# Performance work log

Measured on AMD Instinct MI355X. Metric: run time of the kernel, lower is better.

The kernel has to match this reference:

```python
import jax, jax.numpy as jnp
import numpy as np
from jax import lax

C, CMID, RED, SCALE, KUP, KENC = 128, 64, 8, 2, 5, 3


def _conv(x, w, b=None, pad=0, groups=1):
    y = lax.conv_general_dilated(x, w, (1, 1), [(pad, pad), (pad, pad)],
                                 feature_group_count=groups,
                                 dimension_numbers=('NCHW', 'OIHW', 'NCHW'))
    if b is not None:
        y = y + b[None, :, None, None]
    return y


def setup_inputs() -> dict:
    key = jax.random.key(0)
    ks = jax.random.split(key, 8)
    s = 0.05
    return {
        'X': jax.random.normal(ks[0], (2, C, 64, 64), jnp.float32),
        'w3': jax.random.normal(ks[1], (CMID, C, 3, 3), jnp.float32) * s,
        'b3': jnp.zeros((CMID,), jnp.float32),
        'w5': jax.random.normal(ks[2], (CMID, C, 5, 5), jnp.float32) * s,
        'b5': jnp.zeros((CMID,), jnp.float32),
        'wa1': jax.random.normal(ks[3], (CMID // RED, CMID, 1, 1), jnp.float32) * s,
        'ba1': jnp.zeros((CMID // RED,), jnp.float32),
        'wa2': jax.random.normal(ks[4], (CMID, CMID // RED, 1, 1), jnp.float32) * s,
        'ba2': jnp.zeros((CMID,), jnp.float32),
        'wedge': jax.random.normal(ks[5], (CMID, 1, 3, 3), jnp.float32) * s,
        'wenc': jax.random.normal(ks[6], ((SCALE * KUP) ** 2, CMID, KENC, KENC), jnp.float32) * s,
    }


def reference(X, w3, b3, w5, b5, wa1, ba1, wa2, ba2, wedge, wenc):
    b, c, h, w = X.shape
    h_, w_ = h * SCALE, w * SCALE

    # kernel-prediction branch: 3x3 + 5x5 compression convs
    W = _conv(X, w3, b3, pad=1) + _conv(X, w5, b5, pad=2)

    # DetailEnhanceAttention: SE-style channel gate + depthwise edge conv
    avg = jnp.mean(W, axis=(2, 3), keepdims=True)            # (b, cmid, 1, 1)
    a = _conv(avg, wa1, ba1, pad=0)
    a = jax.nn.sigmoid(_conv(a, wa2, ba2, pad=0))
    edge = _conv(W, wedge, None, pad=1, groups=CMID)          # depthwise 3x3
    W = W * a + edge

    # encoder conv -> (b, (scale*k_up)^2, h, w)
    W = _conv(W, wenc, None, pad=KENC // 2)

    # PixelShuffle(scale): channels (k_up^2, r, r) -> (k_up^2, h*r, w*r)
    Wp = W.reshape(b, KUP * KUP, SCALE, SCALE, h, w)
    Wp = Wp.transpose(0, 1, 4, 2, 5, 3).reshape(b, KUP * KUP, h_, w_)
    Wp = jax.nn.softmax(Wp, axis=1)                           # softmax over k_up^2 taps

    # nearest upsample of X to (b, c, h_, w_)
    Xu = jnp.repeat(jnp.repeat(X, SCALE, axis=2), SCALE, axis=3)

    # unfold: kernel=k_up, dilation=scale, padding=k_up//2*scale
    p = (KUP // 2) * SCALE
    Xpad = jnp.pad(Xu, ((0, 0), (0, 0), (p, p), (p, p)))
    # (b, c, k_up^2, h_, w_), tap index = ki*k_up + kj (torch unfold order)
    patches = jnp.stack([
        Xpad[:, :, i * SCALE:i * SCALE + h_, j * SCALE:j * SCALE + w_]
        for i in range(KUP) for j in range(KUP)
    ], axis=2)

    out = jnp.einsum('bkhw,bckhw->bchw', Wp, patches)
    return out
```

## Files before the change

### kernel.cpp

```cpp
#include <hip/hip_runtime.h>
#include <math.h>

typedef __attribute__((ext_vector_type(2))) _Float16 f16x2;
typedef __attribute__((ext_vector_type(4))) _Float16 f16x4;
typedef __attribute__((ext_vector_type(8))) _Float16 f16x8;
typedef __attribute__((ext_vector_type(4))) float f32x4;

#if __has_builtin(__builtin_amdgcn_fdot2)
#define FDOT2(a, b, c) __builtin_amdgcn_fdot2((a), (b), (c), false)
#else
static __device__ __forceinline__ float FDOT2(f16x2 a, f16x2 b, float c) {
  return c + (float)a[0] * (float)b[0] + (float)a[1] * (float)b[1];
}
#endif

#define XPAD8_B  0
#define WFC_B    2506752
#define WFE_B    2916352
#define WFEATP_B 3045376
#define WEDGET_B 4194304
#define BCOMB_B  4195456
#define AVG_B    4195712

__global__ __launch_bounds__(256) void prep_kernel(
    const float* __restrict__ X,
    const float* __restrict__ w3, const float* __restrict__ b3,
    const float* __restrict__ w5, const float* __restrict__ b5,
    const float* __restrict__ wedge, const float* __restrict__ wenc,
    char* __restrict__ wsb) {
  int idx = blockIdx.x * 256 + threadIdx.x;
  if (idx < 156672) {
    int x = idx % 72;
    int t = idx / 72;
    int y = t % 68;
    int t2 = t / 68;
    int gg = t2 & 15, b = t2 >> 4;
    int yy = y - 2, xx = x - 2;
    bool ok = (yy >= 0 && yy < 64 && xx >= 0 && xx < 64);
    f16x8 h;
#pragma unroll
    for (int j = 0; j < 8; ++j) {
      float v = ok ? X[((b * 128 + gg * 8 + j) << 12) + yy * 64 + xx] : 0.f;
      h[j] = (_Float16)v;
    }
    ((f16x8*)(wsb + XPAD8_B))[idx] = h;
  }
  if (idx < 25600) {
    int l = idx & 63;
    int q = idx >> 6;
    int ntg = q & 3;
    int q2 = q >> 2;
    int cc = q2 & 3;
    int t = q2 >> 2;
    int ky = t / 5, kx = t % 5;
    int oc = ntg * 16 + (l & 15);
    int ci0 = cc * 32 + (l >> 4) * 8;
    f16x8 h;
#pragma unroll
    for (int i = 0; i < 8; ++i) {
      int ci = ci0 + i;
      float v = w5[(oc * 128 + ci) * 25 + t];
      if (ky >= 1 && ky <= 3 && kx >= 1 && kx <= 3)
        v += w3[(oc * 128 + ci) * 9 + (ky - 1) * 3 + (kx - 1)];
      h[i] = (_Float16)v;
    }
    ((f16x8*)(wsb + WFC_B))[idx] = h;
  }
  if (idx < 8064) {
    int l = idx & 63;
    int q = idx >> 6;
    int nt = q % 7;
    int q2 = q / 7;
    int cc = q2 & 1;
    int t = q2 >> 1;
    int oc = nt * 16 + (l & 15);
    int ci0 = cc * 32 + (l >> 4) * 8;
    f16x8 h;
#pragma unroll
    for (int i = 0; i < 8; ++i) {
      float v = (oc < 100) ? wenc[(oc * 64 + ci0 + i) * 9 + t] : 0.f;
      h[i] = (_Float16)v;
    }
    ((f16x8*)(wsb + WFE_B))[idx] = h;
  }
  if (idx < 6272) {
    int plane = idx / 392, p = idx % 392;
    int r, c;
    if (p < 136) {
      r = (p >= 68) ? 65 : 0;
      c = p % 68;
    } else {
      int q = p - 136;
      r = 1 + (q >> 2);
      int cm = q & 3;
      c = (cm == 0) ? 0 : (64 + cm);
    }
    f16x8 z = {(_Float16)0.f, (_Float16)0.f, (_Float16)0.f, (_Float16)0.f,
               (_Float16)0.f, (_Float16)0.f, (_Float16)0.f, (_Float16)0.f};
    *(f16x8*)((_Float16*)(wsb + WFEATP_B) + ((size_t)(plane * 66 + r) * 68 + c) * 8) = z;
  }
  if (idx < 72) {
    int k = idx >> 3, gg = idx & 7;
    f16x8 h;
#pragma unroll
    for (int j = 0; j < 8; ++j) h[j] = (_Float16)wedge[(gg * 8 + j) * 9 + k];
    ((f16x8*)(wsb + WEDGET_B))[idx] = h;
  }
  if (idx < 64) ((float*)(wsb + BCOMB_B))[idx] = b3[idx] + b5[idx];
  if (idx < 128) ((float*)(wsb + AVG_B))[idx] = b3[idx & 63] + b5[idx & 63];
}

__global__ __launch_bounds__(256) void convw_kernel(
    const _Float16* __restrict__ xpad8, const f16x8* __restrict__ wfc,
    const float* __restrict__ bcomb, _Float16* __restrict__ wfeatp,
    float* __restrict__ avg) {
  __shared__ __attribute__((aligned(16))) _Float16 xs[16 * 776];
  __shared__ float red[2][64][4];
  __shared__ float redm[2][16];
  const int tid = threadIdx.x;
  const int z = blockIdx.z;
  const int b = z >> 2, ntg = z & 3;
  const int tx0 = blockIdx.x * 8, ty0 = blockIdx.y * 4;

  for (int u = tid; u < 1536; u += 256) {
    int gg = u / 96;
    int rem = u - gg * 96;
    int r = rem / 12, c = rem - r * 12;
    f16x8 v = *(const f16x8*)&xpad8[((size_t)((b * 16 + gg) * 68 + ty0 + r) * 72 + tx0 + c) * 8];
    *(f16x8*)&xs[gg * 776 + r * 96 + c * 8] = v;
  }
  __syncthreads();

  const int w = __builtin_amdgcn_readfirstlane(tid >> 6);
  const int l = tid & 63;
  const int pg = w & 1, kh = w >> 1;
  const int lm = l & 15, lg = l >> 4;
  const int p = pg * 16 + lm;
  const int abase = (p >> 3) * 96 + (p & 7) * 8;

  f32x4 acc = {0.f, 0.f, 0.f, 0.f};
  for (int dy = 0; dy < 5; ++dy) {
    for (int dx = 0; dx < 5; ++dx) {
      const int t = dy * 5 + dx;
      const int toff = abase + dy * 96 + dx * 8;
#pragma unroll
      for (int cc2 = 0; cc2 < 2; ++cc2) {
        const int cc = kh * 2 + cc2;
        f16x8 a = *(const f16x8*)&xs[(cc * 4 + lg) * 776 + toff];
        f16x8 bb = wfc[((t * 4 + cc) * 4 + ntg) * 64 + l];
        acc = __builtin_amdgcn_mfma_f32_16x16x32_f16(a, bb, acc, 0, 0, 0);
      }
    }
  }

  if (kh == 1) {
#pragma unroll
    for (int r = 0; r < 4; ++r) red[pg][l][r] = acc[r];
  }
  __syncthreads();
  if (kh == 0) {
#pragma unroll
    for (int r = 0; r < 4; ++r) acc[r] += red[pg][l][r];
    float s = acc[0] + acc[1] + acc[2] + acc[3];
    s += __shfl_xor(s, 16);
    s += __shfl_xor(s, 32);
    if (lg == 0) redm[pg][lm] = s;
    const float bias = bcomb[ntg * 16 + lm];
#pragma unroll
    for (int r = 0; r < 4; ++r) {
      int pd = pg * 16 + lg * 4 + r;
      xs[pd * 24 + lm] = (_Float16)(acc[r] + bias);
    }
  }
  __syncthreads();
  if (tid < 64) {
    int pd = tid >> 1, g2 = tid & 1;
    f16x8 v = *(const f16x8*)&xs[pd * 24 + g2 * 8];
    int gy = ty0 + (pd >> 3), gx = tx0 + (pd & 7);
    *(f16x8*)&wfeatp[((size_t)((b * 8 + ntg * 2 + g2) * 66 + 1 + gy) * 68 + 1 + gx) * 8] = v;
  }
  if (tid < 16) {
    float tot = redm[0][tid] + redm[1][tid];
    atomicAdd(&avg[b * 64 + ntg * 16 + tid], tot * (1.f / 4096.f));
  }
}

#define SM_XT  0
#define SM_XSV 19968
#define SM_TS  25216
#define SM_SML 25216
#define SM_SMW 32640
#define SM_WED 36480
#define SM_TLA 37632
#define SM_GSH 37664
#define SM_TOT 37920

__global__ __launch_bounds__(512) void enccarafe_kernel(
    const _Float16* __restrict__ wfeatp, const f16x8* __restrict__ wfe,
    const _Float16* __restrict__ xpad8, const f16x8* __restrict__ wedgeT,
    const float* __restrict__ wa1, const float* __restrict__ ba1,
    const float* __restrict__ wa2, const float* __restrict__ ba2,
    const float* __restrict__ avg, float* __restrict__ out) {
  __shared__ __attribute__((aligned(16))) char smem[SM_TOT];
  _Float16* xt = (_Float16*)(smem + SM_XT);
  _Float16* xsv = (_Float16*)(smem + SM_XSV);
  _Float16* ts = (_Float16*)(smem + SM_TS);
  float* sml = (float*)(smem + SM_SML);
  f16x2* smw2 = (f16x2*)(smem + SM_SMW);
  f16x8* wedt = (f16x8*)(smem + SM_WED);
  float* tlat = (float*)(smem + SM_TLA);
  float* gsh = (float*)(smem + SM_GSH);

  const int tid = threadIdx.x;
  const int b = blockIdx.z;
  const int tx0 = blockIdx.x * 8, ty0 = blockIdx.y * 2;

  for (int u = tid; u < 1248; u += 512) {
    int gg = u / 78;
    int rem = u - gg * 78;
    int r = rem / 13, c = rem - r * 13;
    f16x8 v = *(const f16x8*)&xpad8[((size_t)((b * 16 + gg) * 68 + ty0 + r) * 72 + tx0 + c) * 8];
    *(f16x8*)&xt[gg * 624 + r * 104 + c * 8] = v;
  }
  for (int u = tid; u < 576; u += 512) {
    int gg = u / 72;
    int rem = u - gg * 72;
    int r = rem / 12, c = rem - r * 12;
    int pr = ty0 - 1 + r, pc = tx0 - 1 + c;
    f16x8 v = {(_Float16)0.f, (_Float16)0.f, (_Float16)0.f, (_Float16)0.f,
               (_Float16)0.f, (_Float16)0.f, (_Float16)0.f, (_Float16)0.f};
    if (pr >= 0 && pr < 66 && pc >= 0 && pc < 68)
      v = *(const f16x8*)&wfeatp[((size_t)((b * 8 + gg) * 66 + pr) * 68 + pc) * 8];
    *(f16x8*)&ts[gg * 584 + r * 96 + c * 8] = v;
  }
  if (tid < 72) wedt[tid] = wedgeT[tid];
  if (tid < 8) {
    float s = ba1[tid];
    for (int i = 0; i < 64; ++i) s += wa1[tid * 64 + i] * avg[b * 64 + i];
    tlat[tid] = s;
  }
  __syncthreads();
  if (tid < 64) {
    float s = ba2[tid];
#pragma unroll
    for (int j = 0; j < 8; ++j) s += wa2[tid * 8 + j] * tlat[j];
    gsh[tid] = 1.f / (1.f + expf(-s));
  }
  __syncthreads();

  if (tid < 320) {
    int gg = tid / 40;
    int rem = tid - gg * 40;
    int r6 = rem / 10, c10 = rem - r6 * 10;
    int vy = ty0 - 1 + r6, vx = tx0 - 1 + c10;
    f16x8 res = {(_Float16)0.f, (_Float16)0.f, (_Float16)0.f, (_Float16)0.f,
                 (_Float16)0.f, (_Float16)0.f, (_Float16)0.f, (_Float16)0.f};
    if (vy >= 0 && vy < 64 && vx >= 0 && vx < 64) {
      float vout[8];
      f16x8 ctr = *(const f16x8*)&ts[gg * 584 + (r6 + 1) * 96 + (c10 + 1) * 8];
#pragma unroll
      for (int j = 0; j < 8; ++j) vout[j] = (float)ctr[j] * gsh[gg * 8 + j];
#pragma unroll
      for (int ky = 0; ky < 3; ++ky) {
#pragma unroll
        for (int kx = 0; kx < 3; ++kx) {
          int k = ky * 3 + kx;
          f16x8 tv = *(const f16x8*)&ts[gg * 584 + (r6 + ky) * 96 + (c10 + kx) * 8];
          f16x8 wv = wedt[k * 8 + gg];
#pragma unroll
          for (int j = 0; j < 8; ++j) vout[j] = fmaf((float)wv[j], (float)tv[j], vout[j]);
        }
      }
#pragma unroll
      for (int j = 0; j < 8; ++j) res[j] = (_Float16)vout[j];
    }
    *(f16x8*)&xsv[gg * 328 + r6 * 80 + c10 * 8] = res;
  }
  __syncthreads();

  {
    const int w = __builtin_amdgcn_readfirstlane(tid >> 6);
    const int l = tid & 63;
    if (w < 7) {
      const int nt = w;
      const int lm = l & 15, lg = l >> 4;
      const int abase = (lm >> 3) * 80 + (lm & 7) * 8;

      f32x4 a0 = {0.f, 0.f, 0.f, 0.f};
      for (int dy = 0; dy < 3; ++dy) {
        for (int dx = 0; dx < 3; ++dx) {
          const int t = dy * 3 + dx;
          const int toff = abase + dy * 80 + dx * 8;
#pragma unroll
          for (int cc = 0; cc < 2; ++cc) {
            f16x8 a = *(const f16x8*)&xsv[(cc * 4 + lg) * 328 + toff];
            f16x8 b0 = wfe[((t * 2 + cc) * 7 + nt) * 64 + l];
            a0 = __builtin_amdgcn_mfma_f32_16x16x32_f16(a, b0, a0, 0, 0, 0);
          }
        }
      }
#pragma unroll
      for (int r = 0; r < 4; ++r)
        sml[(4 * lg + r) * 116 + nt * 16 + lm] = a0[r];
    }
  }
  __syncthreads();

  if (tid < 64) {
    int pix = tid >> 2, sub = tid & 3;
    float lv[25];
    float m = -1e30f;
#pragma unroll
    for (int k = 0; k < 25; ++k) {
      lv[k] = sml[pix * 116 + k * 4 + sub];
      m = fmaxf(m, lv[k]);
    }
    float s = 0.f;
#pragma unroll
    for (int k = 0; k < 25; ++k) {
      lv[k] = __expf(lv[k] - m);
      s += lv[k];
    }
    float inv = 1.f / s;
#pragma unroll
    for (int ki = 0; ki < 5; ++ki) {
#pragma unroll
      for (int pr = 0; pr < 3; ++pr) {
        float wlo = lv[ki * 5 + 2 * pr] * inv;
        float whi = (2 * pr + 1 < 5) ? lv[ki * 5 + 2 * pr + 1] * inv : 0.f;
        f16x2 pk = {(_Float16)wlo, (_Float16)whi};
        smw2[((ki * 3 + pr) * 16 + pix) * 4 + sub] = pk;
      }
    }
  }
  __syncthreads();

  {
    const int slot = tid >> 5;
    const int rem = tid & 31;
    const int syh = rem >> 4, pix = rem & 15;
    const int py = pix >> 3, px = pix & 7;
    const _Float16* xb = xt + slot * 624;

    float acc[2][8];
#pragma unroll
    for (int s = 0; s < 2; ++s)
#pragma unroll
      for (int j = 0; j < 8; ++j) acc[s][j] = 0.f;

    union U8 { f16x8 v; unsigned int u[4]; };
#pragma unroll
    for (int ki = 0; ki < 5; ++ki) {
      const _Float16* row = xb + (py + ki) * 104 + px * 8;
      U8 C[6];
#pragma unroll
      for (int c = 0; c < 6; ++c) C[c].v = *(const f16x8*)(row + c * 8);
#pragma unroll
      for (int pr = 0; pr < 3; ++pr) {
        const f16x2* wp = &smw2[((ki * 3 + pr) * 16 + pix) * 4 + syh * 2];
        f16x2 w0 = wp[0], w1 = wp[1];
        const U8& A = C[2 * pr];
        const U8& B = C[2 * pr + 1];
#pragma unroll
        for (int k = 0; k < 4; ++k) {
          unsigned int lo = __builtin_amdgcn_perm(B.u[k], A.u[k], 0x05040100u);
          unsigned int hi = __builtin_amdgcn_perm(B.u[k], A.u[k], 0x07060302u);
          f16x2 xlo = __builtin_bit_cast(f16x2, lo);
          f16x2 xhi = __builtin_bit_cast(f16x2, hi);
          acc[0][2 * k] = FDOT2(w0, xlo, acc[0][2 * k]);
          acc[1][2 * k] = FDOT2(w1, xlo, acc[1][2 * k]);
          acc[0][2 * k + 1] = FDOT2(w0, xhi, acc[0][2 * k + 1]);
          acc[1][2 * k + 1] = FDOT2(w1, xhi, acc[1][2 * k + 1]);
        }
      }
    }
    int y0o = 2 * (ty0 + py) + syh, x0o = 2 * (tx0 + px);
#pragma unroll
    for (int j = 0; j < 8; ++j) {
      int c = slot * 8 + j;
      float* op = out + ((size_t)(b * 128 + c) * 128 + y0o) * 128 + x0o;
      float2 v0 = {acc[0][j], acc[1][j]};
      *(float2*)op = v0;
    }
  }
}

extern "C" void kernel_launch(void* const* d_in, const int* in_sizes, int n_in,
                              void* d_out, int out_size, void* d_ws, size_t ws_size,
                              hipStream_t stream) {
  const float* X     = (const float*)d_in[0];
  const float* w3    = (const float*)d_in[1];
  const float* b3    = (const float*)d_in[2];
  const float* w5    = (const float*)d_in[3];
  const float* b5    = (const float*)d_in[4];
  const float* wa1   = (const float*)d_in[5];
  const float* ba1   = (const float*)d_in[6];
  const float* wa2   = (const float*)d_in[7];
  const float* ba2   = (const float*)d_in[8];
  const float* wedge = (const float*)d_in[9];
  const float* wenc  = (const float*)d_in[10];
  char* wsb = (char*)d_ws;
  float* out = (float*)d_out;

  _Float16* xpad8  = (_Float16*)(wsb + XPAD8_B);
  f16x8*    wfc    = (f16x8*)(wsb + WFC_B);
  f16x8*    wfe    = (f16x8*)(wsb + WFE_B);
  _Float16* wfeatp = (_Float16*)(wsb + WFEATP_B);
  f16x8*    wedgeT = (f16x8*)(wsb + WEDGET_B);
  float*    bcomb  = (float*)(wsb + BCOMB_B);
  float*    avg    = (float*)(wsb + AVG_B);

  prep_kernel<<<612, 256, 0, stream>>>(X, w3, b3, w5, b5, wedge, wenc, wsb);
  convw_kernel<<<dim3(8, 16, 8), 256, 0, stream>>>(xpad8, wfc, bcomb, wfeatp, avg);
  enccarafe_kernel<<<dim3(8, 32, 2), 512, 0, stream>>>(
      wfeatp, wfe, xpad8, wedgeT, wa1, ba1, wa2, ba2, avg, out);
}
```

Baseline: 42.16 us.

## Split enccarafe blocks across output channel halves with 256 threads each

The final fused encoder+CARAFE kernel now launches twice as many blocks of 256 threads, each handling half of the 128 output channels (cq selects which 64). Each block stages only its half of the padded X tile in shared memory, which cuts LDS usage and should allow more resident blocks. In exchange the edge/attention prologue and the encoder MFMA convolution plus softmax are computed redundantly in both channel-half blocks, and each wave now runs two MFMA accumulators.

```diff
diff --git a/kernel.cpp b/kernel.cpp
--- a/kernel.cpp
+++ b/kernel.cpp
@@ -186,16 +186,16 @@
 }
 
 #define SM_XT  0
-#define SM_XSV 19968
-#define SM_TS  25216
-#define SM_SML 25216
-#define SM_SMW 32640
-#define SM_WED 36480
-#define SM_TLA 37632
-#define SM_GSH 37664
-#define SM_TOT 37920
-
-__global__ __launch_bounds__(512) void enccarafe_kernel(
+#define SM_XSV 9984
+#define SM_TS  15232
+#define SM_SML 15232
+#define SM_SMW 22656
+#define SM_WED 26496
+#define SM_TLA 27648
+#define SM_GSH 27680
+#define SM_TOT 27936
+
+__global__ __launch_bounds__(256) void enccarafe_kernel(
     const _Float16* __restrict__ wfeatp, const f16x8* __restrict__ wfe,
     const _Float16* __restrict__ xpad8, const f16x8* __restrict__ wedgeT,
     const float* __restrict__ wa1, const float* __restrict__ ba1,
@@ -212,17 +212,18 @@
   float* gsh = (float*)(smem + SM_GSH);
 
   const int tid = threadIdx.x;
-  const int b = blockIdx.z;
+  const int z = blockIdx.z;
+  const int b = z >> 1, cq = z & 1;
   const int tx0 = blockIdx.x * 8, ty0 = blockIdx.y * 2;
 
-  for (int u = tid; u < 1248; u += 512) {
+  for (int u = tid; u < 624; u += 256) {
     int gg = u / 78;
     int rem = u - gg * 78;
     int r = rem / 13, c = rem - r * 13;
-    f16x8 v = *(const f16x8*)&xpad8[((size_t)((b * 16 + gg) * 68 + ty0 + r) * 72 + tx0 + c) * 8];
+    f16x8 v = *(const f16x8*)&xpad8[((size_t)((b * 16 + cq * 8 + gg) * 68 + ty0 + r) * 72 + tx0 + c) * 8];
     *(f16x8*)&xt[gg * 624 + r * 104 + c * 8] = v;
   }
-  for (int u = tid; u < 576; u += 512) {
+  for (int u = tid; u < 576; u += 256) {
     int gg = u / 72;
     int rem = u - gg * 72;
     int r = rem / 12, c = rem - r * 12;
@@ -248,9 +249,9 @@
   }
   __syncthreads();
 
-  if (tid < 320) {
-    int gg = tid / 40;
-    int rem = tid - gg * 40;
+  for (int u = tid; u < 320; u += 256) {
+    int gg = u / 40;
+    int rem = u - gg * 40;
     int r6 = rem / 10, c10 = rem - r6 * 10;
     int vy = ty0 - 1 + r6, vx = tx0 - 1 + c10;
     f16x8 res = {(_Float16)0.f, (_Float16)0.f, (_Float16)0.f, (_Float16)0.f,
@@ -281,27 +282,32 @@
   {
     const int w = __builtin_amdgcn_readfirstlane(tid >> 6);
     const int l = tid & 63;
-    if (w < 7) {
-      const int nt = w;
-      const int lm = l & 15, lg = l >> 4;
-      const int abase = (lm >> 3) * 80 + (lm & 7) * 8;
-
-      f32x4 a0 = {0.f, 0.f, 0.f, 0.f};
-      for (int dy = 0; dy < 3; ++dy) {
-        for (int dx = 0; dx < 3; ++dx) {
-          const int t = dy * 3 + dx;
-          const int toff = abase + dy * 80 + dx * 8;
-#pragma unroll
-          for (int cc = 0; cc < 2; ++cc) {
-            f16x8 a = *(const f16x8*)&xsv[(cc * 4 + lg) * 328 + toff];
-            f16x8 b0 = wfe[((t * 2 + cc) * 7 + nt) * 64 + l];
-            a0 = __builtin_amdgcn_mfma_f32_16x16x32_f16(a, b0, a0, 0, 0, 0);
+    const int lm = l & 15, lg = l >> 4;
+    const int abase = (lm >> 3) * 80 + (lm & 7) * 8;
+    const int nt0 = w * 2;
+    const int ncnt = (w == 3) ? 1 : 2;
+
+    f32x4 a0 = {0.f, 0.f, 0.f, 0.f}, a1 = {0.f, 0.f, 0.f, 0.f};
+    for (int dy = 0; dy < 3; ++dy) {
+      for (int dx = 0; dx < 3; ++dx) {
+        const int t = dy * 3 + dx;
+        const int toff = abase + dy * 80 + dx * 8;
+#pragma unroll
+        for (int cc = 0; cc < 2; ++cc) {
+          f16x8 a = *(const f16x8*)&xsv[(cc * 4 + lg) * 328 + toff];
+          f16x8 b0 = wfe[((t * 2 + cc) * 7 + nt0) * 64 + l];
+          a0 = __builtin_amdgcn_mfma_f32_16x16x32_f16(a, b0, a0, 0, 0, 0);
+          if (ncnt == 2) {
+            f16x8 b1 = wfe[((t * 2 + cc) * 7 + nt0 + 1) * 64 + l];
+            a1 = __builtin_amdgcn_mfma_f32_16x16x32_f16(a, b1, a1, 0, 0, 0);
           }
         }
       }
-#pragma unroll
-      for (int r = 0; r < 4; ++r)
-        sml[(4 * lg + r) * 116 + nt * 16 + lm] = a0[r];
+    }
+#pragma unroll
+    for (int r = 0; r < 4; ++r) {
+      sml[(4 * lg + r) * 116 + nt0 * 16 + lm] = a0[r];
+      if (ncnt == 2) sml[(4 * lg + r) * 116 + (nt0 + 1) * 16 + lm] = a1[r];
     }
   }
   __syncthreads();
@@ -377,7 +383,7 @@
     int y0o = 2 * (ty0 + py) + syh, x0o = 2 * (tx0 + px);
 #pragma unroll
     for (int j = 0; j < 8; ++j) {
-      int c = slot * 8 + j;
+      int c = cq * 64 + slot * 8 + j;
       float* op = out + ((size_t)(b * 128 + c) * 128 + y0o) * 128 + x0o;
       float2 v0 = {acc[0][j], acc[1][j]};
       *(float2*)op = v0;
@@ -412,6 +418,6 @@
 
   prep_kernel<<<612, 256, 0, stream>>>(X, w3, b3, w5, b5, wedge, wenc, wsb);
   convw_kernel<<<dim3(8, 16, 8), 256, 0, stream>>>(xpad8, wfc, bcomb, wfeatp, avg);
-  enccarafe_kernel<<<dim3(8, 32, 2), 512, 0, stream>>>(
+  enccarafe_kernel<<<dim3(8, 32, 4), 256, 0, stream>>>(
       wfeatp, wfe, xpad8, wedgeT, wa1, ba1, wa2, ba2, avg, out);
 }
```

Measured after the change: 49.96 us. 1.18x slower.

## Fuse three kernels into one persistent kernel with software grid barriers

Applied to the files above, without the earlier changes.

Merges the prep, compression-conv and encoder/CARAFE kernels into a single 512-block launch separated by atomic-counter grid barriers, with a memset to reset the barrier counter. Each block of the conv phase handles two former 256-thread tiles. The aim is to remove kernel launch gaps and inter-kernel drain between stages. In exchange it adds a memset launch and spin-wait barriers, and it relies on all 512 blocks being co-resident (launch_bounds 512,4 with about 54KB of LDS); if they are not, the kernel deadlocks.

```diff
diff --git a/kernel.cpp b/kernel.cpp
--- a/kernel.cpp
+++ b/kernel.cpp
@@ -21,168 +21,23 @@
 #define WEDGET_B 4194304
 #define BCOMB_B  4195456
 #define AVG_B    4195712
-
-__global__ __launch_bounds__(256) void prep_kernel(
-    const float* __restrict__ X,
-    const float* __restrict__ w3, const float* __restrict__ b3,
-    const float* __restrict__ w5, const float* __restrict__ b5,
-    const float* __restrict__ wedge, const float* __restrict__ wenc,
-    char* __restrict__ wsb) {
-  int idx = blockIdx.x * 256 + threadIdx.x;
-  if (idx < 156672) {
-    int x = idx % 72;
-    int t = idx / 72;
-    int y = t % 68;
-    int t2 = t / 68;
-    int gg = t2 & 15, b = t2 >> 4;
-    int yy = y - 2, xx = x - 2;
-    bool ok = (yy >= 0 && yy < 64 && xx >= 0 && xx < 64);
-    f16x8 h;
-#pragma unroll
-    for (int j = 0; j < 8; ++j) {
-      float v = ok ? X[((b * 128 + gg * 8 + j) << 12) + yy * 64 + xx] : 0.f;
-      h[j] = (_Float16)v;
-    }
-    ((f16x8*)(wsb + XPAD8_B))[idx] = h;
-  }
-  if (idx < 25600) {
-    int l = idx & 63;
-    int q = idx >> 6;
-    int ntg = q & 3;
-    int q2 = q >> 2;
-    int cc = q2 & 3;
-    int t = q2 >> 2;
-    int ky = t / 5, kx = t % 5;
-    int oc = ntg * 16 + (l & 15);
-    int ci0 = cc * 32 + (l >> 4) * 8;
-    f16x8 h;
-#pragma unroll
-    for (int i = 0; i < 8; ++i) {
-      int ci = ci0 + i;
-      float v = w5[(oc * 128 + ci) * 25 + t];
-      if (ky >= 1 && ky <= 3 && kx >= 1 && kx <= 3)
-        v += w3[(oc * 128 + ci) * 9 + (ky - 1) * 3 + (kx - 1)];
-      h[i] = (_Float16)v;
-    }
-    ((f16x8*)(wsb + WFC_B))[idx] = h;
-  }
-  if (idx < 8064) {
-    int l = idx & 63;
-    int q = idx >> 6;
-    int nt = q % 7;
-    int q2 = q / 7;
-    int cc = q2 & 1;
-    int t = q2 >> 1;
-    int oc = nt * 16 + (l & 15);
-    int ci0 = cc * 32 + (l >> 4) * 8;
-    f16x8 h;
-#pragma unroll
-    for (int i = 0; i < 8; ++i) {
-      float v = (oc < 100) ? wenc[(oc * 64 + ci0 + i) * 9 + t] : 0.f;
-      h[i] = (_Float16)v;
-    }
-    ((f16x8*)(wsb + WFE_B))[idx] = h;
-  }
-  if (idx < 6272) {
-    int plane = idx / 392, p = idx % 392;
-    int r, c;
-    if (p < 136) {
-      r = (p >= 68) ? 65 : 0;
-      c = p % 68;
+#define BAR_B    4196224
+
+static __device__ __forceinline__ void grid_barrier(unsigned int* bar, unsigned int nb) {
+  __syncthreads();
+  if (threadIdx.x == 0) {
+    __threadfence();
+    unsigned int g = atomicAdd(bar + 1, 0u);
+    if (atomicAdd(bar, 1u) == nb - 1) {
+      atomicExch(bar, 0u);
+      __threadfence();
+      atomicAdd(bar + 1, 1u);
     } else {
-      int q = p - 136;
-      r = 1 + (q >> 2);
-      int cm = q & 3;
-      c = (cm == 0) ? 0 : (64 + cm);
-    }
-    f16x8 z = {(_Float16)0.f, (_Float16)0.f, (_Float16)0.f, (_Float16)0.f,
-               (_Float16)0.f, (_Float16)0.f, (_Float16)0.f, (_Float16)0.f};
-    *(f16x8*)((_Float16*)(wsb + WFEATP_B) + ((size_t)(plane * 66 + r) * 68 + c) * 8) = z;
-  }
-  if (idx < 72) {
-    int k = idx >> 3, gg = idx & 7;
-    f16x8 h;
-#pragma unroll
-    for (int j = 0; j < 8; ++j) h[j] = (_Float16)wedge[(gg * 8 + j) * 9 + k];
-    ((f16x8*)(wsb + WEDGET_B))[idx] = h;
-  }
-  if (idx < 64) ((float*)(wsb + BCOMB_B))[idx] = b3[idx] + b5[idx];
-  if (idx < 128) ((float*)(wsb + AVG_B))[idx] = b3[idx & 63] + b5[idx & 63];
-}
-
-__global__ __launch_bounds__(256) void convw_kernel(
-    const _Float16* __restrict__ xpad8, const f16x8* __restrict__ wfc,
-    const float* __restrict__ bcomb, _Float16* __restrict__ wfeatp,
-    float* __restrict__ avg) {
-  __shared__ __attribute__((aligned(16))) _Float16 xs[16 * 776];
-  __shared__ float red[2][64][4];
-  __shared__ float redm[2][16];
-  const int tid = threadIdx.x;
-  const int z = blockIdx.z;
-  const int b = z >> 2, ntg = z & 3;
-  const int tx0 = blockIdx.x * 8, ty0 = blockIdx.y * 4;
-
-  for (int u = tid; u < 1536; u += 256) {
-    int gg = u / 96;
-    int rem = u - gg * 96;
-    int r = rem / 12, c = rem - r * 12;
-    f16x8 v = *(const f16x8*)&xpad8[((size_t)((b * 16 + gg) * 68 + ty0 + r) * 72 + tx0 + c) * 8];
-    *(f16x8*)&xs[gg * 776 + r * 96 + c * 8] = v;
+      while (atomicAdd(bar + 1, 0u) == g) __builtin_amdgcn_s_sleep(8);
+      __threadfence();
+    }
   }
   __syncthreads();
-
-  const int w = __builtin_amdgcn_readfirstlane(tid >> 6);
-  const int l = tid & 63;
-  const int pg = w & 1, kh = w >> 1;
-  const int lm = l & 15, lg = l >> 4;
-  const int p = pg * 16 + lm;
-  const int abase = (p >> 3) * 96 + (p & 7) * 8;
-
-  f32x4 acc = {0.f, 0.f, 0.f, 0.f};
-  for (int dy = 0; dy < 5; ++dy) {
-    for (int dx = 0; dx < 5; ++dx) {
-      const int t = dy * 5 + dx;
-      const int toff = abase + dy * 96 + dx * 8;
-#pragma unroll
-      for (int cc2 = 0; cc2 < 2; ++cc2) {
-        const int cc = kh * 2 + cc2;
-        f16x8 a = *(const f16x8*)&xs[(cc * 4 + lg) * 776 + toff];
-        f16x8 bb = wfc[((t * 4 + cc) * 4 + ntg) * 64 + l];
-        acc = __builtin_amdgcn_mfma_f32_16x16x32_f16(a, bb, acc, 0, 0, 0);
-      }
-    }
-  }
-
-  if (kh == 1) {
-#pragma unroll
-    for (int r = 0; r < 4; ++r) red[pg][l][r] = acc[r];
-  }
-  __syncthreads();
-  if (kh == 0) {
-#pragma unroll
-    for (int r = 0; r < 4; ++r) acc[r] += red[pg][l][r];
-    float s = acc[0] + acc[1] + acc[2] + acc[3];
-    s += __shfl_xor(s, 16);
-    s += __shfl_xor(s, 32);
-    if (lg == 0) redm[pg][lm] = s;
-    const float bias = bcomb[ntg * 16 + lm];
-#pragma unroll
-    for (int r = 0; r < 4; ++r) {
-      int pd = pg * 16 + lg * 4 + r;
-      xs[pd * 24 + lm] = (_Float16)(acc[r] + bias);
-    }
-  }
-  __syncthreads();
-  if (tid < 64) {
-    int pd = tid >> 1, g2 = tid & 1;
-    f16x8 v = *(const f16x8*)&xs[pd * 24 + g2 * 8];
-    int gy = ty0 + (pd >> 3), gx = tx0 + (pd & 7);
-    *(f16x8*)&wfeatp[((size_t)((b * 8 + ntg * 2 + g2) * 66 + 1 + gy) * 68 + 1 + gx) * 8] = v;
-  }
-  if (tid < 16) {
-    float tot = redm[0][tid] + redm[1][tid];
-    atomicAdd(&avg[b * 64 + ntg * 16 + tid], tot * (1.f / 4096.f));
-  }
 }
 
 #define SM_XT  0
@@ -193,194 +48,372 @@
 #define SM_WED 36480
 #define SM_TLA 37632
 #define SM_GSH 37664
-#define SM_TOT 37920
-
-__global__ __launch_bounds__(512) void enccarafe_kernel(
-    const _Float16* __restrict__ wfeatp, const f16x8* __restrict__ wfe,
-    const _Float16* __restrict__ xpad8, const f16x8* __restrict__ wedgeT,
-    const float* __restrict__ wa1, const float* __restrict__ ba1,
-    const float* __restrict__ wa2, const float* __restrict__ ba2,
-    const float* __restrict__ avg, float* __restrict__ out) {
-  __shared__ __attribute__((aligned(16))) char smem[SM_TOT];
-  _Float16* xt = (_Float16*)(smem + SM_XT);
-  _Float16* xsv = (_Float16*)(smem + SM_XSV);
-  _Float16* ts = (_Float16*)(smem + SM_TS);
-  float* sml = (float*)(smem + SM_SML);
-  f16x2* smw2 = (f16x2*)(smem + SM_SMW);
-  f16x8* wedt = (f16x8*)(smem + SM_WED);
-  float* tlat = (float*)(smem + SM_TLA);
-  float* gsh = (float*)(smem + SM_GSH);
-
+#define SMEM_BYTES 54272
+
+__global__ __launch_bounds__(512, 4) void fused_kernel(
+    const float* __restrict__ X, const float* __restrict__ w3,
+    const float* __restrict__ b3, const float* __restrict__ w5,
+    const float* __restrict__ b5, const float* __restrict__ wa1,
+    const float* __restrict__ ba1, const float* __restrict__ wa2,
+    const float* __restrict__ ba2, const float* __restrict__ wedge,
+    const float* __restrict__ wenc, char* __restrict__ wsb,
+    float* __restrict__ out) {
+  __shared__ __attribute__((aligned(16))) char SMEM[SMEM_BYTES];
   const int tid = threadIdx.x;
-  const int b = blockIdx.z;
-  const int tx0 = blockIdx.x * 8, ty0 = blockIdx.y * 2;
-
-  for (int u = tid; u < 1248; u += 512) {
-    int gg = u / 78;
-    int rem = u - gg * 78;
-    int r = rem / 13, c = rem - r * 13;
-    f16x8 v = *(const f16x8*)&xpad8[((size_t)((b * 16 + gg) * 68 + ty0 + r) * 72 + tx0 + c) * 8];
-    *(f16x8*)&xt[gg * 624 + r * 104 + c * 8] = v;
+  const int bid = blockIdx.x;
+  unsigned int* bar = (unsigned int*)(wsb + BAR_B);
+
+  {
+    const int idx = bid * 512 + tid;
+    if (idx < 156672) {
+      int x = idx % 72;
+      int t = idx / 72;
+      int y = t % 68;
+      int t2 = t / 68;
+      int gg = t2 & 15, b = t2 >> 4;
+      int yy = y - 2, xx = x - 2;
+      bool ok = (yy >= 0 && yy < 64 && xx >= 0 && xx < 64);
+      f16x8 h;
+#pragma unroll
+      for (int j = 0; j < 8; ++j) {
+        float v = ok ? X[((b * 128 + gg * 8 + j) << 12) + yy * 64 + xx] : 0.f;
+        h[j] = (_Float16)v;
+      }
+      ((f16x8*)(wsb + XPAD8_B))[idx] = h;
+    }
+    if (idx < 25600) {
+      int l = idx & 63;
+      int q = idx >> 6;
+      int ntg = q & 3;
+      int q2 = q >> 2;
+      int cc = q2 & 3;
+      int t = q2 >> 2;
+      int ky = t / 5, kx = t % 5;
+      int oc = ntg * 16 + (l & 15);
+      int ci0 = cc * 32 + (l >> 4) * 8;
+      f16x8 h;
+#pragma unroll
+      for (int i = 0; i < 8; ++i) {
+        int ci = ci0 + i;
+        float v = w5[(oc * 128 + ci) * 25 + t];
+        if (ky >= 1 && ky <= 3 && kx >= 1 && kx <= 3)
+          v += w3[(oc * 128 + ci) * 9 + (ky - 1) * 3 + (kx - 1)];
+        h[i] = (_Float16)v;
+      }
+      ((f16x8*)(wsb + WFC_B))[idx] = h;
+    }
+    if (idx < 8064) {
+      int l = idx & 63;
+      int q = idx >> 6;
+      int nt = q % 7;
+      int q2 = q / 7;
+      int cc = q2 & 1;
+      int t = q2 >> 1;
+      int oc = nt * 16 + (l & 15);
+      int ci0 = cc * 32 + (l >> 4) * 8;
+      f16x8 h;
+#pragma unroll
+      for (int i = 0; i < 8; ++i) {
+        float v = (oc < 100) ? wenc[(oc * 64 + ci0 + i) * 9 + t] : 0.f;
+        h[i] = (_Float16)v;
+      }
+      ((f16x8*)(wsb + WFE_B))[idx] = h;
+    }
+    if (idx < 6272) {
+      int plane = idx / 392, p = idx % 392;
+      int r, c;
+      if (p < 136) {
+        r = (p >= 68) ? 65 : 0;
+        c = p % 68;
+      } else {
+        int q = p - 136;
+        r = 1 + (q >> 2);
+        int cm = q & 3;
+        c = (cm == 0) ? 0 : (64 + cm);
+      }
+      f16x8 z = {(_Float16)0.f, (_Float16)0.f, (_Float16)0.f, (_Float16)0.f,
+                 (_Float16)0.f, (_Float16)0.f, (_Float16)0.f, (_Float16)0.f};
+      *(f16x8*)((_Float16*)(wsb + WFEATP_B) + ((size_t)(plane * 66 + r) * 68 + c) * 8) = z;
+    }
+    if (idx < 72) {
+      int k = idx >> 3, gg = idx & 7;
+      f16x8 h;
+#pragma unroll
+      for (int j = 0; j < 8; ++j) h[j] = (_Float16)wedge[(gg * 8 + j) * 9 + k];
+      ((f16x8*)(wsb + WEDGET_B))[idx] = h;
+    }
+    if (idx < 64) ((float*)(wsb + BCOMB_B))[idx] = b3[idx] + b5[idx];
+    if (idx < 128) ((float*)(wsb + AVG_B))[idx] = b3[idx & 63] + b5[idx & 63];
   }
-  for (int u = tid; u < 576; u += 512) {
-    int gg = u / 72;
-    int rem = u - gg * 72;
-    int r = rem / 12, c = rem - r * 12;
-    int pr = ty0 - 1 + r, pc = tx0 - 1 + c;
-    f16x8 v = {(_Float16)0.f, (_Float16)0.f, (_Float16)0.f, (_Float16)0.f,
-               (_Float16)0.f, (_Float16)0.f, (_Float16)0.f, (_Float16)0.f};
-    if (pr >= 0 && pr < 66 && pc >= 0 && pc < 68)
-      v = *(const f16x8*)&wfeatp[((size_t)((b * 8 + gg) * 66 + pr) * 68 + pc) * 8];
-    *(f16x8*)&ts[gg * 584 + r * 96 + c * 8] = v;
+  grid_barrier(bar, 512);
+
+  {
+    const _Float16* xpad8 = (const _Float16*)(wsb + XPAD8_B);
+    const f16x8* wfc = (const f16x8*)(wsb + WFC_B);
+    const float* bcomb = (const float*)(wsb + BCOMB_B);
+    _Float16* wfeatp = (_Float16*)(wsb + WFEATP_B);
+    float* avg = (float*)(wsb + AVG_B);
+
+    const int half = tid >> 8;
+    const int t2 = tid & 255;
+    const int u = bid * 2 + half;
+    const int bx = u & 7, by = (u >> 3) & 15, zz = u >> 7;
+    const int b = zz >> 2, ntg = zz & 3;
+    const int tx0 = bx * 8, ty0 = by * 4;
+    _Float16* xs = (_Float16*)(SMEM + half * 24832);
+    float* red = (float*)(SMEM + 49664 + half * 2048);
+    float* redm = (float*)(SMEM + 53760 + half * 128);
+
+    for (int uu = t2; uu < 1536; uu += 256) {
+      int gg = uu / 96;
+      int rem = uu - gg * 96;
+      int r = rem / 12, c = rem - r * 12;
+      f16x8 v = *(const f16x8*)&xpad8[((size_t)((b * 16 + gg) * 68 + ty0 + r) * 72 + tx0 + c) * 8];
+      *(f16x8*)&xs[gg * 776 + r * 96 + c * 8] = v;
+    }
+    __syncthreads();
+
+    const int w = __builtin_amdgcn_readfirstlane(t2 >> 6);
+    const int l = t2 & 63;
+    const int pg = w & 1, kh = w >> 1;
+    const int lm = l & 15, lg = l >> 4;
+    const int p = pg * 16 + lm;
+    const int abase = (p >> 3) * 96 + (p & 7) * 8;
+
+    f32x4 acc = {0.f, 0.f, 0.f, 0.f};
+    for (int dy = 0; dy < 5; ++dy) {
+      for (int dx = 0; dx < 5; ++dx) {
+        const int t = dy * 5 + dx;
+        const int toff = abase + dy * 96 + dx * 8;
+#pragma unroll
+        for (int cc2 = 0; cc2 < 2; ++cc2) {
+          const int cc = kh * 2 + cc2;
+          f16x8 a = *(const f16x8*)&xs[(cc * 4 + lg) * 776 + toff];
+          f16x8 bb = wfc[((t * 4 + cc) * 4 + ntg) * 64 + l];
+          acc = __builtin_amdgcn_mfma_f32_16x16x32_f16(a, bb, acc, 0, 0, 0);
+        }
+      }
+    }
+
+    if (kh == 1) {
+#pragma unroll
+      for (int r = 0; r < 4; ++r) red[(pg * 64 + l) * 4 + r] = acc[r];
+    }
+    __syncthreads();
+    if (kh == 0) {
+#pragma unroll
+      for (int r = 0; r < 4; ++r) acc[r] += red[(pg * 64 + l) * 4 + r];
+      float s = acc[0] + acc[1] + acc[2] + acc[3];
+      s += __shfl_xor(s, 16);
+      s += __shfl_xor(s, 32);
+      if (lg == 0) redm[pg * 16 + lm] = s;
+      const float bias = bcomb[ntg * 16 + lm];
+#pragma unroll
+      for (int r = 0; r < 4; ++r) {
+        int pd = pg * 16 + lg * 4 + r;
+        xs[pd * 24 + lm] = (_Float16)(acc[r] + bias);
+      }
+    }
+    __syncthreads();
+    if (t2 < 64) {
+      int pd = t2 >> 1, g2 = t2 & 1;
+      f16x8 v = *(const f16x8*)&xs[pd * 24 + g2 * 8];
+      int gy = ty0 + (pd >> 3), gx = tx0 + (pd & 7);
+      *(f16x8*)&wfeatp[((size_t)((b * 8 + ntg * 2 + g2) * 66 + 1 + gy) * 68 + 1 + gx) * 8] = v;
+    }
+    if (t2 < 16) {
+      float tot = redm[t2] + redm[16 + t2];
+      atomicAdd(&avg[b * 64 + ntg * 16 + t2], tot * (1.f / 4096.f));
+    }
   }
-  if (tid < 72) wedt[tid] = wedgeT[tid];
-  if (tid < 8) {
-    float s = ba1[tid];
-    for (int i = 0; i < 64; ++i) s += wa1[tid * 64 + i] * avg[b * 64 + i];
-    tlat[tid] = s;
-  }
-  __syncthreads();
-  if (tid < 64) {
-    float s = ba2[tid];
-#pragma unroll
-    for (int j = 0; j < 8; ++j) s += wa2[tid * 8 + j] * tlat[j];
-    gsh[tid] = 1.f / (1.f + expf(-s));
-  }
-  __syncthreads();
-
-  if (tid < 320) {
-    int gg = tid / 40;
-    int rem = tid - gg * 40;
-    int r6 = rem / 10, c10 = rem - r6 * 10;
-    int vy = ty0 - 1 + r6, vx = tx0 - 1 + c10;
-    f16x8 res = {(_Float16)0.f, (_Float16)0.f, (_Float16)0.f, (_Float16)0.f,
+  grid_barrier(bar, 512);
+
+  {
+    const _Float16* wfeatp = (const _Float16*)(wsb + WFEATP_B);
+    const f16x8* wfe = (const f16x8*)(wsb + WFE_B);
+    const _Float16* xpad8 = (const _Float16*)(wsb + XPAD8_B);
+    const f16x8* wedgeT = (const f16x8*)(wsb + WEDGET_B);
+    const float* avg = (const float*)(wsb + AVG_B);
+
+    _Float16* xt = (_Float16*)(SMEM + SM_XT);
+    _Float16* xsv = (_Float16*)(SMEM + SM_XSV);
+    _Float16* ts = (_Float16*)(SMEM + SM_TS);
+    float* sml = (float*)(SMEM + SM_SML);
+    f16x2* smw2 = (f16x2*)(SMEM + SM_SMW);
+    f16x8* wedt = (f16x8*)(SMEM + SM_WED);
+    float* tlat = (float*)(SMEM + SM_TLA);
+    float* gsh = (float*)(SMEM + SM_GSH);
+
+    const int bx = bid & 7, by = (bid >> 3) & 31, b = bid >> 8;
+    const int tx0 = bx * 8, ty0 = by * 2;
+
+    for (int u = tid; u < 1248; u += 512) {
+      int gg = u / 78;
+      int rem = u - gg * 78;
+      int r = rem / 13, c = rem - r * 13;
+      f16x8 v = *(const f16x8*)&xpad8[((size_t)((b * 16 + gg) * 68 + ty0 + r) * 72 + tx0 + c) * 8];
+      *(f16x8*)&xt[gg * 624 + r * 104 + c * 8] = v;
+    }
+    for (int u = tid; u < 576; u += 512) {
+      int gg = u / 72;
+      int rem = u - gg * 72;
+      int r = rem / 12, c = rem - r * 12;
+      int pr = ty0 - 1 + r, pc = tx0 - 1 + c;
+      f16x8 v = {(_Float16)0.f, (_Float16)0.f, (_Float16)0.f, (_Float16)0.f,
                  (_Float16)0.f, (_Float16)0.f, (_Float16)0.f, (_Float16)0.f};
-    if (vy >= 0 && vy < 64 && vx >= 0 && vx < 64) {
-      float vout[8];
-      f16x8 ctr = *(const f16x8*)&ts[gg * 584 + (r6 + 1) * 96 + (c10 + 1) * 8];
-#pragma unroll
-      for (int j = 0; j < 8; ++j) vout[j] = (float)ctr[j] * gsh[gg * 8 + j];
-#pragma unroll
-      for (int ky = 0; ky < 3; ++ky) {
-#pragma unroll
-        for (int kx = 0; kx < 3; ++kx) {
-          int k = ky * 3 + kx;
-          f16x8 tv = *(const f16x8*)&ts[gg * 584 + (r6 + ky) * 96 + (c10 + kx) * 8];
-          f16x8 wv = wedt[k * 8 + gg];
-#pragma unroll
-          for (int j = 0; j < 8; ++j) vout[j] = fmaf((float)wv[j], (float)tv[j], vout[j]);
-        }
-      }
-#pragma unroll
-      for (int j = 0; j < 8; ++j) res[j] = (_Float16)vout[j];
-    }
-    *(f16x8*)&xsv[gg * 328 + r6 * 80 + c10 * 8] = res;
-  }
-  __syncthreads();
-
-  {
-    const int w = __builtin_amdgcn_readfirstlane(tid >> 6);
-    const int l = tid & 63;
-    if (w < 7) {
-      const int nt = w;
-      const int lm = l & 15, lg = l >> 4;
-      const int abase = (lm >> 3) * 80 + (lm & 7) * 8;
-
-      f32x4 a0 = {0.f, 0.f, 0.f, 0.f};
-      for (int dy = 0; dy < 3; ++dy) {
-        for (int dx = 0; dx < 3; ++dx) {
-          const int t = dy * 3 + dx;
-          const int toff = abase + dy * 80 + dx * 8;
-#pragma unroll
-          for (int cc = 0; cc < 2; ++cc) {
-            f16x8 a = *(const f16x8*)&xsv[(cc * 4 + lg) * 328 + toff];
-            f16x8 b0 = wfe[((t * 2 + cc) * 7 + nt) * 64 + l];
-            a0 = __builtin_amdgcn_mfma_f32_16x16x32_f16(a, b0, a0, 0, 0, 0);
+      if (pr >= 0 && pr < 66 && pc >= 0 && pc < 68)
+        v = *(const f16x8*)&wfeatp[((size_t)((b * 8 + gg) * 66 + pr) * 68 + pc) * 8];
+      *(f16x8*)&ts[gg * 584 + r * 96 + c * 8] = v;
+    }
+    if (tid < 72) wedt[tid] = wedgeT[tid];
+    if (tid < 8) {
+      float s = ba1[tid];
+      for (int i = 0; i < 64; ++i) s += wa1[tid * 64 + i] * avg[b * 64 + i];
+      tlat[tid] = s;
+    }
+    __syncthreads();
+    if (tid < 64) {
+      float s = ba2[tid];
+#pragma unroll
+      for (int j = 0; j < 8; ++j) s += wa2[tid * 8 + j] * tlat[j];
+      gsh[tid] = 1.f / (1.f + expf(-s));
+    }
+    __syncthreads();
+
+    if (tid < 320) {
+      int gg = tid / 40;
+      int rem = tid - gg * 40;
+      int r6 = rem / 10, c10 = rem - r6 * 10;
+      int vy = ty0 - 1 + r6, vx = tx0 - 1 + c10;
+      f16x8 res = {(_Float16)0.f, (_Float16)0.f, (_Float16)0.f, (_Float16)0.f,
+                   (_Float16)0.f, (_Float16)0.f, (_Float16)0.f, (_Float16)0.f};
+      if (vy >= 0 && vy < 64 && vx >= 0 && vx < 64) {
+        float vout[8];
+        f16x8 ctr = *(const f16x8*)&ts[gg * 584 + (r6 + 1) * 96 + (c10 + 1) * 8];
+#pragma unroll
+        for (int j = 0; j < 8; ++j) vout[j] = (float)ctr[j] * gsh[gg * 8 + j];
+#pragma unroll
+        for (int ky = 0; ky < 3; ++ky) {
+#pragma unroll
+          for (int kx = 0; kx < 3; ++kx) {
+            int k = ky * 3 + kx;
+            f16x8 tv = *(const f16x8*)&ts[gg * 584 + (r6 + ky) * 96 + (c10 + kx) * 8];
+            f16x8 wv = wedt[k * 8 + gg];
+#pragma unroll
+            for (int j = 0; j < 8; ++j) vout[j] = fmaf((float)wv[j], (float)tv[j], vout[j]);
           }
         }
-      }
-#pragma unroll
-      for (int r = 0; r < 4; ++r)
-        sml[(4 * lg + r) * 116 + nt * 16 + lm] = a0[r];
-    }
-  }
-  __syncthreads();
-
-  if (tid < 64) {
-    int pix = tid >> 2, sub = tid & 3;
-    float lv[25];
-    float m = -1e30f;
-#pragma unroll
-    for (int k = 0; k < 25; ++k) {
-      lv[k] = sml[pix * 116 + k * 4 + sub];
-      m = fmaxf(m, lv[k]);
-    }
-    float s = 0.f;
-#pragma unroll
-    for (int k = 0; k < 25; ++k) {
-      lv[k] = __expf(lv[k] - m);
-      s += lv[k];
-    }
-    float inv = 1.f / s;
-#pragma unroll
-    for (int ki = 0; ki < 5; ++ki) {
-#pragma unroll
-      for (int pr = 0; pr < 3; ++pr) {
-        float wlo = lv[ki * 5 + 2 * pr] * inv;
-        float whi = (2 * pr + 1 < 5) ? lv[ki * 5 + 2 * pr + 1] * inv : 0.f;
-        f16x2 pk = {(_Float16)wlo, (_Float16)whi};
-        smw2[((ki * 3 + pr) * 16 + pix) * 4 + sub] = pk;
-      }
-    }
-  }
-  __syncthreads();
-
-  {
-    const int slot = tid >> 5;
-    const int rem = tid & 31;
-    const int syh = rem >> 4, pix = rem & 15;
-    const int py = pix >> 3, px = pix & 7;
-    const _Float16* xb = xt + slot * 624;
-
-    float acc[2][8];
-#pragma unroll
-    for (int s = 0; s < 2; ++s)
-#pragma unroll
-      for (int j = 0; j < 8; ++j) acc[s][j] = 0.f;
-
-    union U8 { f16x8 v; unsigned int u[4]; };
-#pragma unroll
-    for (int ki = 0; ki < 5; ++ki) {
-      const _Float16* row = xb + (py + ki) * 104 + px * 8;
-      U8 C[6];
-#pragma unroll
-      for (int c = 0; c < 6; ++c) C[c].v = *(const f16x8*)(row + c * 8);
-#pragma unroll
-      for (int pr = 0; pr < 3; ++pr) {
-        const f16x2* wp = &smw2[((ki * 3 + pr) * 16 + pix) * 4 + syh * 2];
-        f16x2 w0 = wp[0], w1 = wp[1];
-        const U8& A = C[2 * pr];
-        const U8& B = C[2 * pr + 1];
-#pragma unroll
-        for (int k = 0; k < 4; ++k) {
-          unsigned int lo = __builtin_amdgcn_perm(B.u[k], A.u[k], 0x05040100u);
-          unsigned int hi = __builtin_amdgcn_perm(B.u[k], A.u[k], 0x07060302u);
-          f16x2 xlo = __builtin_bit_cast(f16x2, lo);
-          f16x2 xhi = __builtin_bit_cast(f16x2, hi);
-          acc[0][2 * k] = FDOT2(w0, xlo, acc[0][2 * k]);
-          acc[1][2 * k] = FDOT2(w1, xlo, acc[1][2 * k]);
-          acc[0][2 * k + 1] = FDOT2(w0, xhi, acc[0][2 * k + 1]);
-          acc[1][2 * k + 1] = FDOT2(w1, xhi, acc[1][2 * k + 1]);
+#pragma unroll
+        for (int j = 0; j < 8; ++j) res[j] = (_Float16)vout[j];
+      }
+      *(f16x8*)&xsv[gg * 328 + r6 * 80 + c10 * 8] = res;
+    }
+    __syncthreads();
+
+    {
+      const int w = __builtin_amdgcn_readfirstlane(tid >> 6);
+      const int l = tid & 63;
+      if (w < 7) {
+        const int nt = w;
+        const int lm = l & 15, lg = l >> 4;
+        const int abase = (lm >> 3) * 80 + (lm & 7) * 8;
+
+        f32x4 a0 = {0.f, 0.f, 0.f, 0.f};
+        for (int dy = 0; dy < 3; ++dy) {
+          for (int dx = 0; dx < 3; ++dx) {
+            const int t = dy * 3 + dx;
+            const int toff = abase + dy * 80 + dx * 8;
+#pragma unroll
+            for (int cc = 0; cc < 2; ++cc) {
+              f16x8 a = *(const f16x8*)&xsv[(cc * 4 + lg) * 328 + toff];
+              f16x8 b0 = wfe[((t * 2 + cc) * 7 + nt) * 64 + l];
+              a0 = __builtin_amdgcn_mfma_f32_16x16x32_f16(a, b0, a0, 0, 0, 0);
+            }
+          }
         }
-      }
-    }
-    int y0o = 2 * (ty0 + py) + syh, x0o = 2 * (tx0 + px);
-#pragma unroll
-    for (int j = 0; j < 8; ++j) {
-      int c = slot * 8 + j;
-      float* op = out + ((size_t)(b * 128 + c) * 128 + y0o) * 128 + x0o;
-      float2 v0 = {acc[0][j], acc[1][j]};
-      *(float2*)op = v0;
+#pragma unroll
+        for (int r = 0; r < 4; ++r)
+          sml[(4 * lg + r) * 116 + nt * 16 + lm] = a0[r];
+      }
+    }
+    __syncthreads();
+
+    if (tid < 64) {
+      int pix = tid >> 2, sub = tid & 3;
+      float lv[25];
+      float m = -1e30f;
+#pragma unroll
+      for (int k = 0; k < 25; ++k) {
+        lv[k] = sml[pix * 116 + k * 4 + sub];
+        m = fmaxf(m, lv[k]);
+      }
+      float s = 0.f;
+#pragma unroll
+      for (int k = 0; k < 25; ++k) {
+        lv[k] = __expf(lv[k] - m);
+        s += lv[k];
+      }
+      float inv = 1.f / s;
+#pragma unroll
+      for (int ki = 0; ki < 5; ++ki) {
+#pragma unroll
+        for (int pr = 0; pr < 3; ++pr) {
+          float wlo = lv[ki * 5 + 2 * pr] * inv;
+          float whi = (2 * pr + 1 < 5) ? lv[ki * 5 + 2 * pr + 1] * inv : 0.f;
+          f16x2 pk = {(_Float16)wlo, (_Float16)whi};
+          smw2[((ki * 3 + pr) * 16 + pix) * 4 + sub] = pk;
+        }
+      }
+    }
+    __syncthreads();
+
+    {
+      const int slot = tid >> 5;
+      const int rem = tid & 31;
+      const int syh = rem >> 4, pix = rem & 15;
+      const int py = pix >> 3, px = pix & 7;
+      const _Float16* xb = xt + slot * 624;
+
+      float acc[2][8];
+#pragma unroll
+      for (int s = 0; s < 2; ++s)
+#pragma unroll
+        for (int j = 0; j < 8; ++j) acc[s][j] = 0.f;
+
+      union U8 { f16x8 v; unsigned int u[4]; };
+#pragma unroll
+      for (int ki = 0; ki < 5; ++ki) {
+        const _Float16* row = xb + (py + ki) * 104 + px * 8;
+        U8 C[6];
+#pragma unroll
+        for (int c = 0; c < 6; ++c) C[c].v = *(const f16x8*)(row + c * 8);
+#pragma unroll
+        for (int pr = 0; pr < 3; ++pr) {
+          const f16x2* wp = &smw2[((ki * 3 + pr) * 16 + pix) * 4 + syh * 2];
+          f16x2 w0 = wp[0], w1 = wp[1];
+          const U8& A = C[2 * pr];
+          const U8& B = C[2 * pr + 1];
+#pragma unroll
+          for (int k = 0; k < 4; ++k) {
+            unsigned int lo = __builtin_amdgcn_perm(B.u[k], A.u[k], 0x05040100u);
+            unsigned int hi = __builtin_amdgcn_perm(B.u[k], A.u[k], 0x07060302u);
+            f16x2 xlo = __builtin_bit_cast(f16x2, lo);
+            f16x2 xhi = __builtin_bit_cast(f16x2, hi);
+            acc[0][2 * k] = FDOT2(w0, xlo, acc[0][2 * k]);
+            acc[1][2 * k] = FDOT2(w1, xlo, acc[1][2 * k]);
+            acc[0][2 * k + 1] = FDOT2(w0, xhi, acc[0][2 * k + 1]);
+            acc[1][2 * k + 1] = FDOT2(w1, xhi, acc[1][2 * k + 1]);
+          }
+        }
+      }
+      int y0o = 2 * (ty0 + py) + syh, x0o = 2 * (tx0 + px);
+#pragma unroll
+      for (int j = 0; j < 8; ++j) {
+        int c = slot * 8 + j;
+        float* op = out + ((size_t)(b * 128 + c) * 128 + y0o) * 128 + x0o;
+        float2 v0 = {acc[0][j], acc[1][j]};
+        *(float2*)op = v0;
+      }
     }
   }
 }
@@ -402,16 +435,7 @@
   char* wsb = (char*)d_ws;
   float* out = (float*)d_out;
 
-  _Float16* xpad8  = (_Float16*)(wsb + XPAD8_B);
-  f16x8*    wfc    = (f16x8*)(wsb + WFC_B);
-  f16x8*    wfe    = (f16x8*)(wsb + WFE_B);
-  _Float16* wfeatp = (_Float16*)(wsb + WFEATP_B);
-  f16x8*    wedgeT = (f16x8*)(wsb + WEDGET_B);
-  float*    bcomb  = (float*)(wsb + BCOMB_B);
-  float*    avg    = (float*)(wsb + AVG_B);
-
-  prep_kernel<<<612, 256, 0, stream>>>(X, w3, b3, w5, b5, wedge, wenc, wsb);
-  convw_kernel<<<dim3(8, 16, 8), 256, 0, stream>>>(xpad8, wfc, bcomb, wfeatp, avg);
-  enccarafe_kernel<<<dim3(8, 32, 2), 512, 0, stream>>>(
-      wfeatp, wfe, xpad8, wedgeT, wa1, ba1, wa2, ba2, avg, out);
+  hipMemsetAsync(wsb + BAR_B, 0, 8, stream);
+  fused_kernel<<<512, 512, 0, stream>>>(X, w3, b3, w5, b5, wa1, ba1, wa2, ba2,
+                                        wedge, wenc, wsb, out);
 }
```

Measured after the change: 165.5 us. 292% more time.
